# Performance work log

Measured on AMD Instinct MI355X. Metric: run time of the kernel, lower is better.

The kernel has to match this reference:

```python
import jax, jax.numpy as jnp
import numpy as np

B, S, W = 16, 512, 5
H, E, V = 512, 256, 100000


def setup_inputs() -> dict:
    key = jax.random.key(0)
    ks = jax.random.split(key, 20)
    inp = {
        "hiddens": jax.random.normal(ks[0], (B, S, H), jnp.float32),
        "masks": jax.random.randint(ks[1], (B, S), 0, 2, jnp.int32),
        "begins": jax.random.randint(ks[2], (B, S, W), 0, V, jnp.int32),
        "begin_lens": jax.random.randint(ks[3], (B, S), 0, W + 1, jnp.int32),
        "middles": jax.random.randint(ks[4], (B, S, W), 0, V, jnp.int32),
        "middle_lens": jax.random.randint(ks[5], (B, S), 0, W + 1, jnp.int32),
        "ends": jax.random.randint(ks[6], (B, S, W), 0, V, jnp.int32),
        "end_lens": jax.random.randint(ks[7], (B, S), 0, W + 1, jnp.int32),
        # parameters
        "emb": jax.random.normal(ks[8], (V, E), jnp.float32) * 0.02,
        "W_hidden": jax.random.normal(ks[9], (H, 3 * H), jnp.float32) * (1.0 / np.sqrt(H)),
        "b_hidden": jnp.zeros((3 * H,), jnp.float32),
        "W_begin": jax.random.normal(ks[10], (E, 2 * H), jnp.float32) * (1.0 / np.sqrt(E)),
        "b_begin": jnp.zeros((2 * H,), jnp.float32),
        "W_middle": jax.random.normal(ks[11], (E, 2 * H), jnp.float32) * (1.0 / np.sqrt(E)),
        "b_middle": jnp.zeros((2 * H,), jnp.float32),
        "W_end": jax.random.normal(ks[12], (E, 2 * H), jnp.float32) * (1.0 / np.sqrt(E)),
        "b_end": jnp.zeros((2 * H,), jnp.float32),
        "W_gate": jax.random.normal(ks[13], (H, 9), jnp.float32) * (1.0 / np.sqrt(H)),
        "b_gate": jnp.zeros((9,), jnp.float32),
    }
    return inp


def _len_mask(lens, w):
    # True where the lattice candidate is valid (mimics _make_mask's 1s)
    return jnp.arange(w)[None, None, :] < lens[:, :, None]


def _gates(hiddens, masks, W_gate, b_gate):
    b, s, _ = hiddens.shape
    lmr = hiddens @ W_gate + b_gate                      # (B,S,9)
    left, mid, right = jnp.split(lmr, 3, axis=-1)        # each (B,S,3)
    g = jax.nn.sigmoid(left[:, :-2] + mid[:, 1:-1] + right[:, 2:])  # (B,S-2,3)
    ones = jnp.ones((b, 1), g.dtype)
    zeros = jnp.zeros((b, 1), g.dtype)
    begin_g = jnp.concatenate([ones, g[..., 0], ones], axis=1)
    mid_g = jnp.concatenate([zeros, g[..., 1], zeros], axis=1)
    end_g = jnp.concatenate([ones, g[..., 2], ones], axis=1)
    pad = masks == 0
    z = jnp.zeros((), g.dtype)
    return (jnp.where(pad, z, begin_g), jnp.where(pad, z, mid_g), jnp.where(pad, z, end_g))


def reference(hiddens, masks, begins, begin_lens, middles, middle_lens, ends, end_lens,
              emb, W_hidden, b_hidden, W_begin, b_begin, W_middle, b_middle,
              W_end, b_end, W_gate, b_gate):
    w = begins.shape[-1]
    begin_m = _len_mask(begin_lens, w)
    middle_m = _len_mask(middle_lens, w)
    end_m = _len_mask(end_lens, w)

    begin_kv = emb[begins] @ W_begin + b_begin           # (B,S,W,2H)
    middle_kv = emb[middles] @ W_middle + b_middle
    end_kv = emb[ends] @ W_end + b_end

    query, hidden_key, hidden_value = jnp.split(hiddens @ W_hidden + b_hidden, 3, axis=-1)
    bg, mg, eg = _gates(hiddens, masks, W_gate, b_gate)
    begin_kv = bg[:, :, None, None] * begin_kv
    middle_kv = mg[:, :, None, None] * middle_kv
    end_kv = eg[:, :, None, None] * end_kv

    kv = jnp.concatenate([begin_kv, middle_kv, end_kv], axis=-2)   # (B,S,3W,2H)
    h = hiddens.shape[-1]
    keys, values = jnp.split(kv, 2, axis=-1)
    keys = jnp.concatenate([hidden_key[:, :, None, :], keys], axis=-2)     # (B,S,1+3W,H)
    values = jnp.concatenate([hidden_value[:, :, None, :], values], axis=-2)

    # combined mask: True entries get -1e10 (faithful to masked_fill_(masks, -1e10))
    score_mask = jnp.concatenate(
        [(masks != 0)[:, :, None], begin_m, middle_m, end_m], axis=-1)     # (B,S,1+3W)

    scores = jnp.einsum("bsh,bskh->bsk", query, keys)
    scores = jnp.where(score_mask, jnp.asarray(-1e10, scores.dtype), scores)
    weights = jax.nn.softmax(scores, axis=-1)
    return jnp.einsum("bsk,bskh->bsh", weights, values)
```

## Files before the change

kernel.cpp:

```cpp
#include <hip/hip_runtime.h>
#include <cstdint>
#include <cstddef>


typedef unsigned short u16;
typedef _Float16 f16;
typedef __attribute__((ext_vector_type(8))) f16 f16x8;
typedef __attribute__((ext_vector_type(4))) float f32x4;

#define MROWS 8192
#define SS 512

static __device__ __forceinline__ u16 f2h(float x) {
  f16 h = (f16)x;
  return __builtin_bit_cast(u16, h);
}
static __device__ __forceinline__ float h2f(u16 h) {
  return (float)__builtin_bit_cast(f16, h);
}
static __device__ __forceinline__ float sigm(float x) { return 1.f / (1.f + __expf(-x)); }

static __device__ __forceinline__ void gl2lds(const u16* g, u16* l) {
  __builtin_amdgcn_global_load_lds(
      (const __attribute__((address_space(1))) unsigned int*)g,
      (__attribute__((address_space(3))) unsigned int*)l, 16, 0, 0);
}

__global__ __launch_bounds__(256) void prep_all(
    const float* __restrict__ X, const float* __restrict__ Wg,
    const float* __restrict__ bg, const float* __restrict__ Wh,
    const float* __restrict__ Wb, const float* __restrict__ Wm,
    const float* __restrict__ We, const float* __restrict__ bb,
    const float* __restrict__ bm, const float* __restrict__ be,
    const float* __restrict__ bh, const int* __restrict__ masks,
    u16* __restrict__ Xh, float* __restrict__ lmr, float* __restrict__ s0,
    u16* __restrict__ Breg, u16* __restrict__ WvT, float* __restrict__ bcat,
    float* __restrict__ u, float* __restrict__ cbuf, int* __restrict__ idx,
    int* __restrict__ perm, int* __restrict__ cnts) {
  __shared__ __align__(16) char smem_raw[32768];
  float* shmem = (float*)smem_raw;
  u16* As = (u16*)smem_raw;
  u16* Bs = (u16*)(smem_raw + 16384);
#define TI(r, c) shmem[(r)*65 + (c)]
  const int b = blockIdx.x;
  const int t = threadIdx.x;
  if (b < 64) {
    int k0 = (b & 7) * 64;
    int n0 = (b >> 3) * 64;
#pragma unroll
    for (int i = 0; i < 16; i++) {
      int li = i * 256 + t; int r = li >> 6, c = li & 63;
      TI(r, c) = Wh[(size_t)(k0 + r) * 1536 + 1024 + n0 + c];
    }
    __syncthreads();
#pragma unroll
    for (int i = 0; i < 16; i++) {
      int li = i * 256 + t; int r = li >> 6, c = li & 63;
      Breg[(size_t)(512 + n0 + r) * 512 + k0 + c] = f2h(TI(c, r));
    }
  } else if (b < 160) {
    int idx2 = b - 64;
    int ty = idx2 >> 5;
    int rem = idx2 & 31;
    int c0 = (rem & 3) * 64;
    int n0 = (rem >> 2) * 64;
    const float* Wsrc = ty == 0 ? Wb : ty == 1 ? Wm : We;
#pragma unroll
    for (int i = 0; i < 16; i++) {
      int li = i * 256 + t; int r = li >> 6, c = li & 63;
      TI(r, c) = Wsrc[(size_t)(c0 + r) * 1024 + 512 + n0 + c];
    }
    __syncthreads();
#pragma unroll
    for (int i = 0; i < 16; i++) {
      int li = i * 256 + t; int r = li >> 6, c = li & 63;
      WvT[(size_t)(n0 + r) * 768 + ty * 256 + c0 + c] = f2h(TI(c, r));
    }
  } else if (b < 516) {
    const int lane = t & 63;
    const int widx = (b - 160) * 4 + (t >> 6);
    const int c = lane * 8;
    if (widx < 896) {
      int n = widx;
      float acc = 0.f;
      if (n < 771) {
        const float* src;
        if (n < 768) {
          int ty = n >> 8, ce = n & 255;
          src = (ty == 0 ? Wb : ty == 1 ? Wm : We) + (size_t)ce * 1024 + c;
        } else {
          int ty = n - 768;
          src = (ty == 0 ? bb : ty == 1 ? bm : be) + c;
        }
        float4 a0 = *(const float4*)src;
        float4 a1 = *(const float4*)(src + 4);
        float4 b0 = *(const float4*)(bh + c);
        float4 b1 = *(const float4*)(bh + c + 4);
        acc = a0.x * b0.x + a0.y * b0.y + a0.z * b0.z + a0.w * b0.w +
              a1.x * b1.x + a1.y * b1.y + a1.z * b1.z + a1.w * b1.w;
      }
#pragma unroll
      for (int o = 32; o > 0; o >>= 1) acc += __shfl_xor(acc, o);
      if (lane == 0) bcat[512 + n] = acc;
    } else if (widx < 1408) {
      int k = widx - 896;
      const float* wr = Wh + (size_t)k * 1536;
      float4 a0 = *(const float4*)(wr + c);
      float4 a1 = *(const float4*)(wr + c + 4);
      float4 a2 = *(const float4*)(wr + 512 + c);
      float4 a3 = *(const float4*)(wr + 512 + c + 4);
      float4 b0 = *(const float4*)(bh + 512 + c);
      float4 b1 = *(const float4*)(bh + 512 + c + 4);
      float4 b2 = *(const float4*)(bh + c);
      float4 b3 = *(const float4*)(bh + c + 4);
      float acc = a0.x * b0.x + a0.y * b0.y + a0.z * b0.z + a0.w * b0.w +
                  a1.x * b1.x + a1.y * b1.y + a1.z * b1.z + a1.w * b1.w +
                  a2.x * b2.x + a2.y * b2.y + a2.z * b2.z + a2.w * b2.w +
                  a3.x * b3.x + a3.y * b3.y + a3.z * b3.z + a3.w * b3.w;
#pragma unroll
      for (int o = 32; o > 0; o >>= 1) acc += __shfl_xor(acc, o);
      if (lane == 0) u[k] = acc;
    } else if (widx == 1408) {
      float4 b0 = *(const float4*)(bh + c);
      float4 b1 = *(const float4*)(bh + c + 4);
      float4 b2 = *(const float4*)(bh + 512 + c);
      float4 b3 = *(const float4*)(bh + 512 + c + 4);
      float acc = b0.x * b2.x + b0.y * b2.y + b0.z * b2.z + b0.w * b2.w +
                  b1.x * b3.x + b1.y * b3.y + b1.z * b3.z + b1.w * b3.w;
#pragma unroll
      for (int o = 32; o > 0; o >>= 1) acc += __shfl_xor(acc, o);
      if (lane == 0) cbuf[0] = acc;
    } else if (widx < 1417) {
      int i = (widx - 1409) * 64 + lane;
      bcat[i] = bh[1024 + i];
    }
  } else if (b < 1028) {
    const int xb = b - 516;
    if (xb < 32) s0[xb * 256 + t] = 0.f;
    for (int i = t; i < 4608; i += 256) shmem[i] = Wg[i];
    __syncthreads();
    const int lane = t & 63, wid = t >> 6;
#pragma unroll
    for (int it = 0; it < 4; it++) {
      int pos = xb * 16 + it * 4 + wid;
      const float* x = X + (size_t)pos * 512 + lane * 8;
      float4 x0 = *(const float4*)x;
      float4 x1 = *(const float4*)(x + 4);
      float xs[8] = {x0.x, x0.y, x0.z, x0.w, x1.x, x1.y, x1.z, x1.w};
      ushort4 h0, h1;
      h0.x = f2h(xs[0]); h0.y = f2h(xs[1]); h0.z = f2h(xs[2]); h0.w = f2h(xs[3]);
      h1.x = f2h(xs[4]); h1.y = f2h(xs[5]); h1.z = f2h(xs[6]); h1.w = f2h(xs[7]);
      ((ushort4*)Xh)[pos * 128 + lane * 2] = h0;
      ((ushort4*)Xh)[pos * 128 + lane * 2 + 1] = h1;
      float p[9];
#pragma unroll
      for (int c = 0; c < 9; c++) p[c] = 0.f;
      const float* wrow = shmem + (lane * 8) * 9;
#pragma unroll
      for (int j = 0; j < 8; j++)
#pragma unroll
        for (int c = 0; c < 9; c++) p[c] += xs[j] * wrow[j * 9 + c];
#pragma unroll
      for (int c = 0; c < 9; c++)
#pragma unroll
        for (int o = 32; o > 0; o >>= 1) p[c] += __shfl_xor(p[c], o);
      if (lane == 0) {
#pragma unroll
        for (int c = 0; c < 9; c++) lmr[(size_t)pos * 9 + c] = p[c] + bg[c];
      }
    }
  } else if (b < 1060) {
    const int lane = t & 63;
    const int pos = (b - 1028) * 256 + t;
    bool is0 = masks[pos] == 0;
    unsigned long long bal = __ballot(is0);
    unsigned long long below = (lane == 0) ? 0ull : (~0ull >> (64 - lane));
    int rank0 = __popcll(bal & below);
    int rank1 = __popcll((~bal) & below);
    int n0w = __popcll(bal);
    int base0 = 0, base1 = 0;
    if (lane == 0) {
      base0 = atomicAdd(&cnts[0], n0w);
      base1 = atomicAdd(&cnts[1], 64 - n0w);
    }
    base0 = __shfl(base0, 0);
    base1 = __shfl(base1, 0);
    int slot = is0 ? (base0 + rank0) : (8191 - (base1 + rank1));
    perm[pos] = slot;
    idx[slot] = pos;
  } else {
    const int b2 = b - 1060;
    const int m0 = (b2 % 11) * 128;
    const int n0 = (b2 / 11) * 128;
    const int lane = t & 63;
    const int wid = t >> 6;
    const int row = t >> 2;
    const int koff = (t & 3) * 8;
    const int lds0 = row * 32 + koff;
    const int lds1 = 2048 + lds0;

    auto asrc = [&](int r) -> const float* {
      if (r < 512) return Wh + (size_t)r * 1536 + 512;
      int n = r - 512;
      if (n < 768)
        return (n < 256 ? Wb : n < 512 ? Wm : We) + (size_t)(n & 255) * 1024;
      if (n < 771) return (n == 768 ? bb : n == 769 ? bm : be);
      return nullptr;
    };
    const float* pa0 = asrc(m0 + row);
    const float* pa1 = asrc(m0 + 64 + row);
    const float* pb0 = Wh + (size_t)(n0 + row) * 1536;
    const float* pb1 = Wh + (size_t)(n0 + 64 + row) * 1536;

    const int wm = (wid & 1) * 64;
    const int wn = (wid >> 1) * 64;
    const int fr = lane & 15;
    const int kq = (lane >> 4) * 8;

    f32x4 acc[4][4];
#pragma unroll
    for (int i = 0; i < 4; i++)
#pragma unroll
      for (int j = 0; j < 4; j++) acc[i][j] = (f32x4){0.f, 0.f, 0.f, 0.f};

    auto cvt8 = [&](const float* p, int col) -> f16x8 {
      f16x8 h{};
      if (p) {
        float4 v0 = *(const float4*)(p + col);
        float4 v1 = *(const float4*)(p + col + 4);
        h[0] = (f16)v0.x; h[1] = (f16)v0.y; h[2] = (f16)v0.z; h[3] = (f16)v0.w;
        h[4] = (f16)v1.x; h[5] = (f16)v1.y; h[6] = (f16)v1.z; h[7] = (f16)v1.w;
      }
      return h;
    };
    auto STAGE = [&](int kb, int buf) {
      *(f16x8*)&As[buf * 4096 + lds0] = cvt8(pa0, kb + koff);
      *(f16x8*)&As[buf * 4096 + lds1] = cvt8(pa1, kb + koff);
      *(f16x8*)&Bs[buf * 4096 + lds0] = cvt8(pb0, kb + koff);
      *(f16x8*)&Bs[buf * 4096 + lds1] = cvt8(pb1, kb + koff);
    };
    auto COMPUTE = [&](int buf) {
      f16x8 av[4], bv[4];
#pragma unroll
      for (int i = 0; i < 4; i++) {
        av[i] = *(const f16x8*)&As[buf * 4096 + (wm + i * 16 + fr) * 32 + kq];
        bv[i] = *(const f16x8*)&Bs[buf * 4096 + (wn + i * 16 + fr) * 32 + kq];
      }
#pragma unroll
      for (int mt = 0; mt < 4; mt++)
#pragma unroll
        for (int nt = 0; nt < 4; nt++)
          acc[mt][nt] = __builtin_amdgcn_mfma_f32_16x16x32_f16(
              av[mt], bv[nt], acc[mt][nt], 0, 0, 0);
    };

    STAGE(0, 0);
    __syncthreads();
    int buf = 0;
    for (int ki = 0; ki < 15; ++ki) {
      STAGE((ki + 1) * 32, buf ^ 1);
      COMPUTE(buf);
      __syncthreads();
      buf ^= 1;
    }
    COMPUTE(buf);

    const int r0 = (lane >> 4) * 4;
#pragma unroll
    for (int mt = 0; mt < 4; mt++)
#pragma unroll
      for (int nt = 0; nt < 4; nt++) {
        int col = n0 + wn + nt * 16 + fr;
#pragma unroll
        for (int r = 0; r < 4; r++) {
          int orow0 = m0 + wm + mt * 16 + r0 + r;
          int orow = orow0 < 512 ? orow0 : orow0 + 512;
          Breg[(size_t)orow * 512 + col] = f2h(acc[mt][nt][r]);
        }
      }
  }
#undef TI
}

template <int MODE>
__global__ __launch_bounds__(256) void gemm_k(
    const u16* __restrict__ A, const u16* __restrict__ Bt,
    const float* __restrict__ ubias, const float* __restrict__ bcat,
    float* __restrict__ Cf, u16* __restrict__ Cb, int Kdim,
    const u16* __restrict__ Xh, float* __restrict__ s0c,
    const int* __restrict__ idx, const int* __restrict__ cnts,
    const float4* __restrict__ sc4, const u16* __restrict__ HPb,
    const float* __restrict__ bb, const float* __restrict__ bm,
    const float* __restrict__ be) {
  constexpr int BROWS = (MODE == 2) ? 64 : 128;
  constexpr int NT = (MODE == 2) ? 2 : 4;
  __shared__ __align__(16) u16 As[2 * 128 * 32];
  __shared__ __align__(16) u16 Bs[2 * BROWS * 32];

  const int t = threadIdx.x;
  const int lane = t & 63;
  const int wid = t >> 6;
  const int m0 = blockIdx.x * 128;
  const int n0 = blockIdx.y * BROWS;

  bool remap = false;
  if constexpr (MODE == 0) {
    const int cnt0 = cnts[0];
    if (blockIdx.y < 4) {
      if (m0 >= cnt0) return;
      remap = true;
    } else if (blockIdx.y >= 8) {
      if (m0 + 128 <= cnt0) return;
      remap = true;
    }
  }

  int ra0 = m0 + (t >> 2), ra1 = m0 + 64 + (t >> 2);
  if (MODE == 0 && remap) { ra0 = idx[ra0]; ra1 = idx[ra1]; }
  const int rb0 = n0 + (t >> 2), rb1 = n0 + 64 + (t >> 2);
  const int koff = (t & 3) * 8;
  const int lds0 = (t >> 2) * 32 + koff;
  const int lds1 = 2048 + lds0;

  const int wm = (wid & 1) * 64;
  const int wn = (wid >> 1) * (NT * 16);
  const int fr = lane & 15;
  const int kq = (lane >> 4) * 8;

  f32x4 acc[4][NT];
#pragma unroll
  for (int i = 0; i < 4; i++)
#pragma unroll
    for (int j = 0; j < NT; j++) acc[i][j] = (f32x4){0.f, 0.f, 0.f, 0.f};

  auto STAGE = [&](int kb, int buf) {
    gl2lds(&A[(size_t)ra0 * Kdim + kb], &As[buf * 4096 + lds0]);
    gl2lds(&A[(size_t)ra1 * Kdim + kb], &As[buf * 4096 + lds1]);
    gl2lds(&Bt[(size_t)rb0 * Kdim + kb], &Bs[buf * (BROWS * 32) + lds0]);
    if constexpr (BROWS == 128)
      gl2lds(&Bt[(size_t)rb1 * Kdim + kb], &Bs[buf * (BROWS * 32) + lds1]);
  };
  auto COMPUTE = [&](int buf) {
    f16x8 av[4], bv[NT];
#pragma unroll
    for (int i = 0; i < 4; i++)
      av[i] = *(const f16x8*)&As[buf * 4096 + (wm + i * 16 + fr) * 32 + kq];
#pragma unroll
    for (int j = 0; j < NT; j++)
      bv[j] = *(const f16x8*)&Bs[buf * (BROWS * 32) + (wn + j * 16 + fr) * 32 + kq];
#pragma unroll
    for (int mt = 0; mt < 4; mt++)
#pragma unroll
      for (int nt = 0; nt < NT; nt++)
        acc[mt][nt] = __builtin_amdgcn_mfma_f32_16x16x32_f16(
            av[mt], bv[nt], acc[mt][nt], 0, 0, 0);
  };

  STAGE(koff, 0);
  __syncthreads();
  const int nk = Kdim >> 5;
  int buf = 0;
  for (int ki = 0; ki < nk - 1; ++ki) {
    STAGE((ki + 1) * 32 + koff, buf ^ 1);
    COMPUTE(buf);
    __syncthreads();
    buf ^= 1;
  }
  COMPUTE(buf);

  const int r0 = (lane >> 4) * 4;
  if constexpr (MODE == 0) {
    if (blockIdx.y < 4) {
      float pl[4][4];
      int xrow[4][4];
#pragma unroll
      for (int mt = 0; mt < 4; mt++)
#pragma unroll
        for (int r = 0; r < 4; r++) {
          pl[mt][r] = 0.f;
          xrow[mt][r] = idx[m0 + wm + mt * 16 + r0 + r];
        }
#pragma unroll
      for (int mt = 0; mt < 4; mt++)
#pragma unroll
        for (int nt = 0; nt < 4; nt++) {
          int col = n0 + wn + nt * 16 + fr;
          float bv2 = ubias[col];
#pragma unroll
          for (int r = 0; r < 4; r++)
            pl[mt][r] += (acc[mt][nt][r] + bv2) *
                         h2f(Xh[(size_t)xrow[mt][r] * 512 + col]);
        }
#pragma unroll
      for (int mt = 0; mt < 4; mt++)
#pragma unroll
        for (int r = 0; r < 4; r++) {
          float p = pl[mt][r];
          p += __shfl_xor(p, 1);
          p += __shfl_xor(p, 2);
          p += __shfl_xor(p, 4);
          p += __shfl_xor(p, 8);
          if (fr == r) {
            int slot = m0 + wm + mt * 16 + r0 + r;
            atomicAdd(&s0c[slot], p);
          }
        }
      return;
    }
    if (blockIdx.y < 8) {
#pragma unroll
      for (int mt = 0; mt < 4; mt++)
#pragma unroll
        for (int nt = 0; nt < 4; nt++) {
          int col = n0 - 512 + wn + nt * 16 + fr;
          float bv2 = bcat[col];
#pragma unroll
          for (int r = 0; r < 4; r++) {
            int row = m0 + wm + mt * 16 + r0 + r;
            Cb[(size_t)row * 1408 + col] = f2h(acc[mt][nt][r] + bv2);
          }
        }
    } else {
#pragma unroll
      for (int mt = 0; mt < 4; mt++)
#pragma unroll
        for (int nt = 0; nt < 4; nt++) {
          int pcol = n0 - 1024 + wn + nt * 16 + fr;
          float bv2 = bcat[512 + pcol];
#pragma unroll
          for (int r = 0; r < 4; r++) {
            int slot = m0 + wm + mt * 16 + r0 + r;
            Cb[(size_t)slot * 1408 + 512 + pcol] = f2h(acc[mt][nt][r] + bv2);
          }
        }
    }
  } else {
#pragma unroll
    for (int mt = 0; mt < 4; mt++)
#pragma unroll
      for (int nt = 0; nt < NT; nt++) {
        int col = n0 + wn + nt * 16 + fr;
        float b0 = bb[512 + col];
        float b1 = bm[512 + col];
        float b2 = be[512 + col];
#pragma unroll
        for (int r = 0; r < 4; r++) {
          int row = m0 + wm + mt * 16 + r0 + r;
          float4 s = sc4[row];
          float hv = h2f(HPb[(size_t)row * 1408 + col]);
          Cf[(size_t)row * 512 + col] =
              s.x * hv + s.y * b0 + s.z * b1 + s.w * b2 + acc[mt][nt][r];
        }
      }
  }
}

__global__ __launch_bounds__(256) void attn_kernel(
    const int* __restrict__ masks, const int* __restrict__ begins,
    const int* __restrict__ blens, const int* __restrict__ middles,
    const int* __restrict__ mlens, const int* __restrict__ ends,
    const int* __restrict__ elens, const float* __restrict__ emb,
    const u16* __restrict__ HPb, const float* __restrict__ lmr,
    const float* __restrict__ s0buf, const float* __restrict__ cbuf,
    const int* __restrict__ perm, float4* __restrict__ sc4,
    u16* __restrict__ Ebar) {
  const int t = threadIdx.x;
  const int lane = t & 63;
  const int wid = t >> 6;
  const int pos = blockIdx.x * 4 + wid;
  const int mask = masks[pos];
  const int slot = perm[pos];
  u16* erow = Ebar + (size_t)pos * 768;

  int l0 = min(blens[pos], 5), l1 = min(mlens[pos], 5), l2 = min(elens[pos], 5);
  int nv = l0 + l1 + l2;

  if (mask == 0) {
    float s0 = s0buf[slot] + cbuf[0];
    int ninv = 15 - nv;
    float w0;
    if (ninv == 0) {
      w0 = 1.f;
    } else {
      float Mx = fmaxf(s0, 0.f);
      float e0 = __expf(s0 - Mx);
      w0 = e0 / (e0 + (float)ninv * __expf(-Mx));
    }
    if (lane == 0) sc4[pos] = make_float4(w0, 0.f, 0.f, 0.f);
    ushort4 zz; zz.x = zz.y = zz.z = zz.w = 0;
    *(ushort4*)(erow + 0 * 256 + lane * 4) = zz;
    *(ushort4*)(erow + 1 * 256 + lane * 4) = zz;
    *(ushort4*)(erow + 2 * 256 + lane * 4) = zz;
  } else {
    const int s = pos & (SS - 1);
    float g[3];
    if (s == 0 || s == SS - 1) {
      g[0] = 1.f; g[1] = 0.f; g[2] = 1.f;
    } else {
      const float* p0 = lmr + (size_t)(pos - 1) * 9;
      const float* p1 = lmr + (size_t)pos * 9;
      const float* p2 = lmr + (size_t)(pos + 1) * 9;
      g[0] = sigm(p0[0] + p1[3] + p2[6]);
      g[1] = sigm(p0[1] + p1[4] + p2[7]);
      g[2] = sigm(p0[2] + p1[5] + p2[8]);
    }
    const bool deg = (nv == 15);
    int l[3] = {l0, l1, l2};
    if (deg) { l[0] = 0; l[1] = 0; l[2] = 0; }

    float4 Pt[3];
    float qb[3];
    if (!deg) {
      const u16* prow = HPb + (size_t)slot * 1408 + 512;
#pragma unroll
      for (int ty = 0; ty < 3; ty++) {
        ushort4 pu = *(const ushort4*)(prow + ty * 256 + lane * 4);
        Pt[ty].x = h2f(pu.x); Pt[ty].y = h2f(pu.y);
        Pt[ty].z = h2f(pu.z); Pt[ty].w = h2f(pu.w);
        qb[ty] = h2f(prow[768 + ty]);
      }
    }
    const int* idxp[3];
    idxp[0] = begins + (size_t)pos * 5;
    idxp[1] = middles + (size_t)pos * 5;
    idxp[2] = ends + (size_t)pos * 5;

    float4 ev[3][5];
    float scv[3][5];
    float Mx = deg ? 0.f : -3.0e38f;
#pragma unroll
    for (int ty = 0; ty < 3; ty++) {
#pragma unroll
      for (int w = 0; w < 5; w++) {
        bool act = (w >= l[ty]);
        if (act) {
          ev[ty][w] = *(const float4*)(emb + (size_t)idxp[ty][w] * 256 + lane * 4);
          float sv = 0.f;
          if (!deg) {
            float4 e = ev[ty][w];
            float d = Pt[ty].x * e.x + Pt[ty].y * e.y + Pt[ty].z * e.z + Pt[ty].w * e.w;
#pragma unroll
            for (int o = 32; o > 0; o >>= 1) d += __shfl_xor(d, o);
            sv = g[ty] * (d + qb[ty]);
          }
          scv[ty][w] = sv;
          Mx = fmaxf(Mx, sv);
        }
      }
    }
    float wts0 = deg ? 1.f : 0.f;
    float zs = wts0;
    float wts[3][5];
#pragma unroll
    for (int ty = 0; ty < 3; ty++)
#pragma unroll
      for (int w = 0; w < 5; w++) {
        bool act = (w >= l[ty]);
        float wv = act ? __expf(scv[ty][w] - Mx) : 0.f;
        wts[ty][w] = wv;
        zs += wv;
      }
    float inv = 1.f / zs;
    float alpha[3];
#pragma unroll
    for (int ty = 0; ty < 3; ty++) {
      float ax = 0.f, ay = 0.f, az = 0.f, aw = 0.f, asum = 0.f;
#pragma unroll
      for (int w = 0; w < 5; w++) {
        if (w >= l[ty]) {
          float wk = wts[ty][w];
          asum += wk;
          ax += wk * ev[ty][w].x;
          ay += wk * ev[ty][w].y;
          az += wk * ev[ty][w].z;
          aw += wk * ev[ty][w].w;
        }
      }
      float sg = g[ty] * inv;
      alpha[ty] = sg * asum;
      ushort4 h;
      h.x = f2h(ax * sg); h.y = f2h(ay * sg); h.z = f2h(az * sg); h.w = f2h(aw * sg);
      *(ushort4*)(erow + ty * 256 + lane * 4) = h;
    }
    if (lane == 0) sc4[pos] = make_float4(wts0 * inv, alpha[0], alpha[1], alpha[2]);
  }
}

extern "C" void kernel_launch(void* const* d_in, const int* in_sizes, int n_in,
                              void* d_out, int out_size, void* d_ws, size_t ws_size,
                              hipStream_t stream) {
  const float* hiddens = (const float*)d_in[0];
  const int* masks = (const int*)d_in[1];
  const int* begins = (const int*)d_in[2];
  const int* blens = (const int*)d_in[3];
  const int* middles = (const int*)d_in[4];
  const int* mlens = (const int*)d_in[5];
  const int* ends = (const int*)d_in[6];
  const int* elens = (const int*)d_in[7];
  const float* emb = (const float*)d_in[8];
  const float* Wh = (const float*)d_in[9];
  const float* bh = (const float*)d_in[10];
  const float* Wb = (const float*)d_in[11];
  const float* bb = (const float*)d_in[12];
  const float* Wm = (const float*)d_in[13];
  const float* bm = (const float*)d_in[14];
  const float* We = (const float*)d_in[15];
  const float* be = (const float*)d_in[16];
  const float* Wg = (const float*)d_in[17];
  const float* bg = (const float*)d_in[18];
  float* out = (float*)d_out;

  char* ws = (char*)d_ws;
  size_t off = 0;
  auto alloc = [&](size_t bytes) -> char* {
    char* p = ws + off;
    off += (bytes + 255) & ~(size_t)255;
    return p;
  };
  u16* Xh = (u16*)alloc((size_t)8192 * 512 * 2);
  u16* Breg = (u16*)alloc((size_t)1920 * 512 * 2);
  u16* WvT = (u16*)alloc((size_t)512 * 768 * 2);
  u16* HPb = (u16*)alloc((size_t)8192 * 1408 * 2);
  float* lmr = (float*)alloc((size_t)8192 * 9 * 4);
  float* s0c = (float*)alloc((size_t)8192 * 4);
  float* bcat = (float*)alloc((size_t)1408 * 4);
  float* u = (float*)alloc((size_t)512 * 4);
  float* cbuf = (float*)alloc((size_t)4);
  float* sc4 = (float*)alloc((size_t)8192 * 4 * 4);
  u16* Ebar = (u16*)alloc((size_t)8192 * 768 * 2);
  int* idx = (int*)alloc((size_t)8192 * 4);
  int* perm = (int*)alloc((size_t)8192 * 4);
  int* cnts = (int*)alloc((size_t)256);
  if (off > ws_size) return;

  hipMemsetAsync(cnts, 0, 8, stream);
  prep_all<<<1104, 256, 0, stream>>>(hiddens, Wg, bg, Wh, Wb, Wm, We, bb, bm, be,
                                     bh, masks, Xh, lmr, s0c, Breg, WvT, bcat,
                                     u, cbuf, idx, perm, cnts);
  gemm_k<0><<<dim3(64, 15), 256, 0, stream>>>(
      Xh, Breg, u, bcat, nullptr, HPb, 512, Xh, s0c, idx, cnts,
      nullptr, nullptr, nullptr, nullptr, nullptr);
  attn_kernel<<<2048, 256, 0, stream>>>(masks, begins, blens, middles, mlens,
                                        ends, elens, emb, HPb, lmr, s0c, cbuf,
                                        perm, (float4*)sc4, Ebar);
  gemm_k<2><<<dim3(64, 8), 256, 0, stream>>>(
      Ebar, WvT, nullptr, nullptr, out, nullptr, 768, nullptr, nullptr,
      nullptr, nullptr, (const float4*)sc4, HPb, bb, bm, be);
}
```

Measured before the change: 303.6 us.

## Fuse all stages into one persistent kernel with software grid barriers

Replaces the four separate kernel launches (prep, projection GEMM, attention, output GEMM) with a single persistent kernel of 512 blocks. Each block loops over the virtual block indices of every stage, and an atomic-counter grid barrier separates the stages. The aim is to remove launch overhead and inter-kernel gaps. In exchange, every block must be co-resident, the barriers add spin cost, and the fixed grid may spread work unevenly across blocks. A timeout inside the barrier can break ordering if residency is not met.

New measurement: 956.9 us. 3.15x slower.

```diff
diff --git a/kernel.cpp b/kernel.cpp
--- a/kernel.cpp
+++ b/kernel.cpp
@@ -8,8 +8,20 @@
 typedef __attribute__((ext_vector_type(8))) f16 f16x8;
 typedef __attribute__((ext_vector_type(4))) float f32x4;
 
-#define MROWS 8192
 #define SS 512
+#define NBLK 512
+
+struct KArgs {
+  const float *X, *Wg, *bg, *Wh, *Wb, *Wm, *We, *bb, *bm, *be, *bh;
+  const int *masks, *begins, *blens, *middles, *mlens, *ends, *elens;
+  const float *emb;
+  u16 *Xh; float *lmr; float *s0c;
+  u16 *Breg, *WvT;
+  float *bcat, *u, *cbuf;
+  int *idx, *perm, *cnts;
+  u16 *HPb; float4 *sc4; u16 *Ebar;
+  float *out;
+};
 
 static __device__ __forceinline__ u16 f2h(float x) {
   f16 h = (f16)x;
@@ -26,23 +38,26 @@
       (__attribute__((address_space(3))) unsigned int*)l, 16, 0, 0);
 }
 
-__global__ __launch_bounds__(256) void prep_all(
-    const float* __restrict__ X, const float* __restrict__ Wg,
-    const float* __restrict__ bg, const float* __restrict__ Wh,
-    const float* __restrict__ Wb, const float* __restrict__ Wm,
-    const float* __restrict__ We, const float* __restrict__ bb,
-    const float* __restrict__ bm, const float* __restrict__ be,
-    const float* __restrict__ bh, const int* __restrict__ masks,
-    u16* __restrict__ Xh, float* __restrict__ lmr, float* __restrict__ s0,
-    u16* __restrict__ Breg, u16* __restrict__ WvT, float* __restrict__ bcat,
-    float* __restrict__ u, float* __restrict__ cbuf, int* __restrict__ idx,
-    int* __restrict__ perm, int* __restrict__ cnts) {
-  __shared__ __align__(16) char smem_raw[32768];
+static __device__ __forceinline__ void gbar(int* ctr) {
+  __syncthreads();
+  __threadfence();
+  if (threadIdx.x == 0) {
+    __hip_atomic_fetch_add(ctr, 1, __ATOMIC_RELEASE, __HIP_MEMORY_SCOPE_AGENT);
+    long long t0 = (long long)__builtin_amdgcn_s_memrealtime();
+    while (__hip_atomic_load(ctr, __ATOMIC_ACQUIRE, __HIP_MEMORY_SCOPE_AGENT) < NBLK) {
+      __builtin_amdgcn_s_sleep(16);
+      if ((long long)__builtin_amdgcn_s_memrealtime() - t0 > 5000000LL) break;
+    }
+  }
+  __syncthreads();
+  __threadfence();
+}
+
+static __device__ void prep_body(int b, const KArgs& A_, char* smem_raw) {
   float* shmem = (float*)smem_raw;
   u16* As = (u16*)smem_raw;
   u16* Bs = (u16*)(smem_raw + 16384);
 #define TI(r, c) shmem[(r)*65 + (c)]
-  const int b = blockIdx.x;
   const int t = threadIdx.x;
   if (b < 64) {
     int k0 = (b & 7) * 64;
@@ -50,13 +65,13 @@
 #pragma unroll
     for (int i = 0; i < 16; i++) {
       int li = i * 256 + t; int r = li >> 6, c = li & 63;
-      TI(r, c) = Wh[(size_t)(k0 + r) * 1536 + 1024 + n0 + c];
+      TI(r, c) = A_.Wh[(size_t)(k0 + r) * 1536 + 1024 + n0 + c];
     }
     __syncthreads();
 #pragma unroll
     for (int i = 0; i < 16; i++) {
       int li = i * 256 + t; int r = li >> 6, c = li & 63;
-      Breg[(size_t)(512 + n0 + r) * 512 + k0 + c] = f2h(TI(c, r));
+      A_.Breg[(size_t)(512 + n0 + r) * 512 + k0 + c] = f2h(TI(c, r));
     }
   } else if (b < 160) {
     int idx2 = b - 64;
@@ -64,7 +79,7 @@
     int rem = idx2 & 31;
     int c0 = (rem & 3) * 64;
     int n0 = (rem >> 2) * 64;
-    const float* Wsrc = ty == 0 ? Wb : ty == 1 ? Wm : We;
+    const float* Wsrc = ty == 0 ? A_.Wb : ty == 1 ? A_.Wm : A_.We;
 #pragma unroll
     for (int i = 0; i < 16; i++) {
       int li = i * 256 + t; int r = li >> 6, c = li & 63;
@@ -74,12 +89,13 @@
 #pragma unroll
     for (int i = 0; i < 16; i++) {
       int li = i * 256 + t; int r = li >> 6, c = li & 63;
-      WvT[(size_t)(n0 + r) * 768 + ty * 256 + c0 + c] = f2h(TI(c, r));
+      A_.WvT[(size_t)(n0 + r) * 768 + ty * 256 + c0 + c] = f2h(TI(c, r));
     }
   } else if (b < 516) {
     const int lane = t & 63;
     const int widx = (b - 160) * 4 + (t >> 6);
     const int c = lane * 8;
+    const float* bh = A_.bh;
     if (widx < 896) {
       int n = widx;
       float acc = 0.f;
@@ -87,10 +103,10 @@
         const float* src;
         if (n < 768) {
           int ty = n >> 8, ce = n & 255;
-          src = (ty == 0 ? Wb : ty == 1 ? Wm : We) + (size_t)ce * 1024 + c;
+          src = (ty == 0 ? A_.Wb : ty == 1 ? A_.Wm : A_.We) + (size_t)ce * 1024 + c;
         } else {
           int ty = n - 768;
-          src = (ty == 0 ? bb : ty == 1 ? bm : be) + c;
+          src = (ty == 0 ? A_.bb : ty == 1 ? A_.bm : A_.be) + c;
         }
         float4 a0 = *(const float4*)src;
         float4 a1 = *(const float4*)(src + 4);
@@ -101,10 +117,10 @@
       }
 #pragma unroll
       for (int o = 32; o > 0; o >>= 1) acc += __shfl_xor(acc, o);
-      if (lane == 0) bcat[512 + n] = acc;
+      if (lane == 0) A_.bcat[512 + n] = acc;
     } else if (widx < 1408) {
       int k = widx - 896;
-      const float* wr = Wh + (size_t)k * 1536;
+      const float* wr = A_.Wh + (size_t)k * 1536;
       float4 a0 = *(const float4*)(wr + c);
       float4 a1 = *(const float4*)(wr + c + 4);
       float4 a2 = *(const float4*)(wr + 512 + c);
@@ -119,7 +135,7 @@
                   a3.x * b3.x + a3.y * b3.y + a3.z * b3.z + a3.w * b3.w;
 #pragma unroll
       for (int o = 32; o > 0; o >>= 1) acc += __shfl_xor(acc, o);
-      if (lane == 0) u[k] = acc;
+      if (lane == 0) A_.u[k] = acc;
     } else if (widx == 1408) {
       float4 b0 = *(const float4*)(bh + c);
       float4 b1 = *(const float4*)(bh + c + 4);
@@ -129,29 +145,29 @@
                   b1.x * b3.x + b1.y * b3.y + b1.z * b3.z + b1.w * b3.w;
 #pragma unroll
       for (int o = 32; o > 0; o >>= 1) acc += __shfl_xor(acc, o);
-      if (lane == 0) cbuf[0] = acc;
+      if (lane == 0) A_.cbuf[0] = acc;
     } else if (widx < 1417) {
       int i = (widx - 1409) * 64 + lane;
-      bcat[i] = bh[1024 + i];
+      A_.bcat[i] = bh[1024 + i];
     }
   } else if (b < 1028) {
     const int xb = b - 516;
-    if (xb < 32) s0[xb * 256 + t] = 0.f;
-    for (int i = t; i < 4608; i += 256) shmem[i] = Wg[i];
+    if (xb < 32) A_.s0c[xb * 256 + t] = 0.f;
+    for (int i = t; i < 4608; i += 256) shmem[i] = A_.Wg[i];
     __syncthreads();
     const int lane = t & 63, wid = t >> 6;
 #pragma unroll
     for (int it = 0; it < 4; it++) {
       int pos = xb * 16 + it * 4 + wid;
-      const float* x = X + (size_t)pos * 512 + lane * 8;
+      const float* x = A_.X + (size_t)pos * 512 + lane * 8;
       float4 x0 = *(const float4*)x;
       float4 x1 = *(const float4*)(x + 4);
       float xs[8] = {x0.x, x0.y, x0.z, x0.w, x1.x, x1.y, x1.z, x1.w};
       ushort4 h0, h1;
       h0.x = f2h(xs[0]); h0.y = f2h(xs[1]); h0.z = f2h(xs[2]); h0.w = f2h(xs[3]);
       h1.x = f2h(xs[4]); h1.y = f2h(xs[5]); h1.z = f2h(xs[6]); h1.w = f2h(xs[7]);
-      ((ushort4*)Xh)[pos * 128 + lane * 2] = h0;
-      ((ushort4*)Xh)[pos * 128 + lane * 2 + 1] = h1;
+      ((ushort4*)A_.Xh)[pos * 128 + lane * 2] = h0;
+      ((ushort4*)A_.Xh)[pos * 128 + lane * 2 + 1] = h1;
       float p[9];
 #pragma unroll
       for (int c = 0; c < 9; c++) p[c] = 0.f;
@@ -166,13 +182,13 @@
         for (int o = 32; o > 0; o >>= 1) p[c] += __shfl_xor(p[c], o);
       if (lane == 0) {
 #pragma unroll
-        for (int c = 0; c < 9; c++) lmr[(size_t)pos * 9 + c] = p[c] + bg[c];
+        for (int c = 0; c < 9; c++) A_.lmr[(size_t)pos * 9 + c] = p[c] + A_.bg[c];
       }
     }
   } else if (b < 1060) {
     const int lane = t & 63;
     const int pos = (b - 1028) * 256 + t;
-    bool is0 = masks[pos] == 0;
+    bool is0 = A_.masks[pos] == 0;
     unsigned long long bal = __ballot(is0);
     unsigned long long below = (lane == 0) ? 0ull : (~0ull >> (64 - lane));
     int rank0 = __popcll(bal & below);
@@ -180,14 +196,14 @@
     int n0w = __popcll(bal);
     int base0 = 0, base1 = 0;
     if (lane == 0) {
-      base0 = atomicAdd(&cnts[0], n0w);
-      base1 = atomicAdd(&cnts[1], 64 - n0w);
+      base0 = atomicAdd(&A_.cnts[0], n0w);
+      base1 = atomicAdd(&A_.cnts[1], 64 - n0w);
     }
     base0 = __shfl(base0, 0);
     base1 = __shfl(base1, 0);
     int slot = is0 ? (base0 + rank0) : (8191 - (base1 + rank1));
-    perm[pos] = slot;
-    idx[slot] = pos;
+    A_.perm[pos] = slot;
+    A_.idx[slot] = pos;
   } else {
     const int b2 = b - 1060;
     const int m0 = (b2 % 11) * 128;
@@ -200,17 +216,17 @@
     const int lds1 = 2048 + lds0;
 
     auto asrc = [&](int r) -> const float* {
-      if (r < 512) return Wh + (size_t)r * 1536 + 512;
+      if (r < 512) return A_.Wh + (size_t)r * 1536 + 512;
       int n = r - 512;
       if (n < 768)
-        return (n < 256 ? Wb : n < 512 ? Wm : We) + (size_t)(n & 255) * 1024;
-      if (n < 771) return (n == 768 ? bb : n == 769 ? bm : be);
+        return (n < 256 ? A_.Wb : n < 512 ? A_.Wm : A_.We) + (size_t)(n & 255) * 1024;
+      if (n < 771) return (n == 768 ? A_.bb : n == 769 ? A_.bm : A_.be);
       return nullptr;
     };
     const float* pa0 = asrc(m0 + row);
     const float* pa1 = asrc(m0 + 64 + row);
-    const float* pb0 = Wh + (size_t)(n0 + row) * 1536;
-    const float* pb1 = Wh + (size_t)(n0 + 64 + row) * 1536;
+    const float* pb0 = A_.Wh + (size_t)(n0 + row) * 1536;
+    const float* pb1 = A_.Wh + (size_t)(n0 + 64 + row) * 1536;
 
     const int wm = (wid & 1) * 64;
     const int wn = (wid >> 1) * 64;
@@ -275,7 +291,7 @@
         for (int r = 0; r < 4; r++) {
           int orow0 = m0 + wm + mt * 16 + r0 + r;
           int orow = orow0 < 512 ? orow0 : orow0 + 512;
-          Breg[(size_t)orow * 512 + col] = f2h(acc[mt][nt][r]);
+          A_.Breg[(size_t)orow * 512 + col] = f2h(acc[mt][nt][r]);
         }
       }
   }
@@ -283,40 +299,35 @@
 }
 
 template <int MODE>
-__global__ __launch_bounds__(256) void gemm_k(
-    const u16* __restrict__ A, const u16* __restrict__ Bt,
-    const float* __restrict__ ubias, const float* __restrict__ bcat,
-    float* __restrict__ Cf, u16* __restrict__ Cb, int Kdim,
-    const u16* __restrict__ Xh, float* __restrict__ s0c,
-    const int* __restrict__ idx, const int* __restrict__ cnts,
-    const float4* __restrict__ sc4, const u16* __restrict__ HPb,
-    const float* __restrict__ bb, const float* __restrict__ bm,
-    const float* __restrict__ be) {
+static __device__ void gemm_body(int bx, int by, const KArgs& A_, char* smem_raw) {
   constexpr int BROWS = (MODE == 2) ? 64 : 128;
   constexpr int NT = (MODE == 2) ? 2 : 4;
-  __shared__ __align__(16) u16 As[2 * 128 * 32];
-  __shared__ __align__(16) u16 Bs[2 * BROWS * 32];
+  constexpr int Kdim = (MODE == 2) ? 768 : 512;
+  u16* As = (u16*)smem_raw;
+  u16* Bs = (u16*)(smem_raw + 16384);
+  const u16* Amat = (MODE == 0) ? A_.Xh : A_.Ebar;
+  const u16* Bt = (MODE == 0) ? A_.Breg : A_.WvT;
 
   const int t = threadIdx.x;
   const int lane = t & 63;
   const int wid = t >> 6;
-  const int m0 = blockIdx.x * 128;
-  const int n0 = blockIdx.y * BROWS;
+  const int m0 = bx * 128;
+  const int n0 = by * BROWS;
 
   bool remap = false;
   if constexpr (MODE == 0) {
-    const int cnt0 = cnts[0];
-    if (blockIdx.y < 4) {
+    const int cnt0 = A_.cnts[0];
+    if (by < 4) {
       if (m0 >= cnt0) return;
       remap = true;
-    } else if (blockIdx.y >= 8) {
+    } else if (by >= 8) {
       if (m0 + 128 <= cnt0) return;
       remap = true;
     }
   }
 
   int ra0 = m0 + (t >> 2), ra1 = m0 + 64 + (t >> 2);
-  if (MODE == 0 && remap) { ra0 = idx[ra0]; ra1 = idx[ra1]; }
+  if (MODE == 0 && remap) { ra0 = A_.idx[ra0]; ra1 = A_.idx[ra1]; }
   const int rb0 = n0 + (t >> 2), rb1 = n0 + 64 + (t >> 2);
   const int koff = (t & 3) * 8;
   const int lds0 = (t >> 2) * 32 + koff;
@@ -334,8 +345,8 @@
     for (int j = 0; j < NT; j++) acc[i][j] = (f32x4){0.f, 0.f, 0.f, 0.f};
 
   auto STAGE = [&](int kb, int buf) {
-    gl2lds(&A[(size_t)ra0 * Kdim + kb], &As[buf * 4096 + lds0]);
-    gl2lds(&A[(size_t)ra1 * Kdim + kb], &As[buf * 4096 + lds1]);
+    gl2lds(&Amat[(size_t)ra0 * Kdim + kb], &As[buf * 4096 + lds0]);
+    gl2lds(&Amat[(size_t)ra1 * Kdim + kb], &As[buf * 4096 + lds1]);
     gl2lds(&Bt[(size_t)rb0 * Kdim + kb], &Bs[buf * (BROWS * 32) + lds0]);
     if constexpr (BROWS == 128)
       gl2lds(&Bt[(size_t)rb1 * Kdim + kb], &Bs[buf * (BROWS * 32) + lds1]);
@@ -358,7 +369,7 @@
 
   STAGE(koff, 0);
   __syncthreads();
-  const int nk = Kdim >> 5;
+  constexpr int nk = Kdim >> 5;
   int buf = 0;
   for (int ki = 0; ki < nk - 1; ++ki) {
     STAGE((ki + 1) * 32 + koff, buf ^ 1);
@@ -370,7 +381,7 @@
 
   const int r0 = (lane >> 4) * 4;
   if constexpr (MODE == 0) {
-    if (blockIdx.y < 4) {
+    if (by < 4) {
       float pl[4][4];
       int xrow[4][4];
 #pragma unroll
@@ -378,18 +389,18 @@
 #pragma unroll
         for (int r = 0; r < 4; r++) {
           pl[mt][r] = 0.f;
-          xrow[mt][r] = idx[m0 + wm + mt * 16 + r0 + r];
+          xrow[mt][r] = A_.idx[m0 + wm + mt * 16 + r0 + r];
         }
 #pragma unroll
       for (int mt = 0; mt < 4; mt++)
 #pragma unroll
         for (int nt = 0; nt < 4; nt++) {
           int col = n0 + wn + nt * 16 + fr;
-          float bv2 = ubias[col];
+          float bv2 = A_.u[col];
 #pragma unroll
           for (int r = 0; r < 4; r++)
             pl[mt][r] += (acc[mt][nt][r] + bv2) *
-                         h2f(Xh[(size_t)xrow[mt][r] * 512 + col]);
+                         h2f(A_.Xh[(size_t)xrow[mt][r] * 512 + col]);
         }
 #pragma unroll
       for (int mt = 0; mt < 4; mt++)
@@ -402,22 +413,22 @@
           p += __shfl_xor(p, 8);
           if (fr == r) {
             int slot = m0 + wm + mt * 16 + r0 + r;
-            atomicAdd(&s0c[slot], p);
+            atomicAdd(&A_.s0c[slot], p);
           }
         }
       return;
     }
-    if (blockIdx.y < 8) {
+    if (by < 8) {
 #pragma unroll
       for (int mt = 0; mt < 4; mt++)
 #pragma unroll
         for (int nt = 0; nt < 4; nt++) {
           int col = n0 - 512 + wn + nt * 16 + fr;
-          float bv2 = bcat[col];
+          float bv2 = A_.bcat[col];
 #pragma unroll
           for (int r = 0; r < 4; r++) {
             int row = m0 + wm + mt * 16 + r0 + r;
-            Cb[(size_t)row * 1408 + col] = f2h(acc[mt][nt][r] + bv2);
+            A_.HPb[(size_t)row * 1408 + col] = f2h(acc[mt][nt][r] + bv2);
           }
         }
     } else {
@@ -426,11 +437,11 @@
 #pragma unroll
         for (int nt = 0; nt < 4; nt++) {
           int pcol = n0 - 1024 + wn + nt * 16 + fr;
-          float bv2 = bcat[512 + pcol];
+          float bv2 = A_.bcat[512 + pcol];
 #pragma unroll
           for (int r = 0; r < 4; r++) {
             int slot = m0 + wm + mt * 16 + r0 + r;
-            Cb[(size_t)slot * 1408 + 512 + pcol] = f2h(acc[mt][nt][r] + bv2);
+            A_.HPb[(size_t)slot * 1408 + 512 + pcol] = f2h(acc[mt][nt][r] + bv2);
           }
         }
     }
@@ -440,43 +451,35 @@
 #pragma unroll
       for (int nt = 0; nt < NT; nt++) {
         int col = n0 + wn + nt * 16 + fr;
-        float b0 = bb[512 + col];
-        float b1 = bm[512 + col];
-        float b2 = be[512 + col];
+        float b0 = A_.bb[512 + col];
+        float b1 = A_.bm[512 + col];
+        float b2 = A_.be[512 + col];
 #pragma unroll
         for (int r = 0; r < 4; r++) {
           int row = m0 + wm + mt * 16 + r0 + r;
-          float4 s = sc4[row];
-          float hv = h2f(HPb[(size_t)row * 1408 + col]);
-          Cf[(size_t)row * 512 + col] =
+          float4 s = A_.sc4[row];
+          float hv = h2f(A_.HPb[(size_t)row * 1408 + col]);
+          A_.out[(size_t)row * 512 + col] =
               s.x * hv + s.y * b0 + s.z * b1 + s.w * b2 + acc[mt][nt][r];
         }
       }
   }
 }
 
-__global__ __launch_bounds__(256) void attn_kernel(
-    const int* __restrict__ masks, const int* __restrict__ begins,
-    const int* __restrict__ blens, const int* __restrict__ middles,
-    const int* __restrict__ mlens, const int* __restrict__ ends,
-    const int* __restrict__ elens, const float* __restrict__ emb,
-    const u16* __restrict__ HPb, const float* __restrict__ lmr,
-    const float* __restrict__ s0buf, const float* __restrict__ cbuf,
-    const int* __restrict__ perm, float4* __restrict__ sc4,
-    u16* __restrict__ Ebar) {
+static __device__ void attn_body(int vb, const KArgs& A_) {
   const int t = threadIdx.x;
   const int lane = t & 63;
   const int wid = t >> 6;
-  const int pos = blockIdx.x * 4 + wid;
-  const int mask = masks[pos];
-  const int slot = perm[pos];
-  u16* erow = Ebar + (size_t)pos * 768;
-
-  int l0 = min(blens[pos], 5), l1 = min(mlens[pos], 5), l2 = min(elens[pos], 5);
+  const int pos = vb * 4 + wid;
+  const int mask = A_.masks[pos];
+  const int slot = A_.perm[pos];
+  u16* erow = A_.Ebar + (size_t)pos * 768;
+
+  int l0 = min(A_.blens[pos], 5), l1 = min(A_.mlens[pos], 5), l2 = min(A_.elens[pos], 5);
   int nv = l0 + l1 + l2;
 
   if (mask == 0) {
-    float s0 = s0buf[slot] + cbuf[0];
+    float s0 = A_.s0c[slot] + A_.cbuf[0];
     int ninv = 15 - nv;
     float w0;
     if (ninv == 0) {
@@ -486,7 +489,7 @@
       float e0 = __expf(s0 - Mx);
       w0 = e0 / (e0 + (float)ninv * __expf(-Mx));
     }
-    if (lane == 0) sc4[pos] = make_float4(w0, 0.f, 0.f, 0.f);
+    if (lane == 0) A_.sc4[pos] = make_float4(w0, 0.f, 0.f, 0.f);
     ushort4 zz; zz.x = zz.y = zz.z = zz.w = 0;
     *(ushort4*)(erow + 0 * 256 + lane * 4) = zz;
     *(ushort4*)(erow + 1 * 256 + lane * 4) = zz;
@@ -497,9 +500,9 @@
     if (s == 0 || s == SS - 1) {
       g[0] = 1.f; g[1] = 0.f; g[2] = 1.f;
     } else {
-      const float* p0 = lmr + (size_t)(pos - 1) * 9;
-      const float* p1 = lmr + (size_t)pos * 9;
-      const float* p2 = lmr + (size_t)(pos + 1) * 9;
+      const float* p0 = A_.lmr + (size_t)(pos - 1) * 9;
+      const float* p1 = A_.lmr + (size_t)pos * 9;
+      const float* p2 = A_.lmr + (size_t)(pos + 1) * 9;
       g[0] = sigm(p0[0] + p1[3] + p2[6]);
       g[1] = sigm(p0[1] + p1[4] + p2[7]);
       g[2] = sigm(p0[2] + p1[5] + p2[8]);
@@ -511,7 +514,7 @@
     float4 Pt[3];
     float qb[3];
     if (!deg) {
-      const u16* prow = HPb + (size_t)slot * 1408 + 512;
+      const u16* prow = A_.HPb + (size_t)slot * 1408 + 512;
 #pragma unroll
       for (int ty = 0; ty < 3; ty++) {
         ushort4 pu = *(const ushort4*)(prow + ty * 256 + lane * 4);
@@ -521,9 +524,9 @@
       }
     }
     const int* idxp[3];
-    idxp[0] = begins + (size_t)pos * 5;
-    idxp[1] = middles + (size_t)pos * 5;
-    idxp[2] = ends + (size_t)pos * 5;
+    idxp[0] = A_.begins + (size_t)pos * 5;
+    idxp[1] = A_.middles + (size_t)pos * 5;
+    idxp[2] = A_.ends + (size_t)pos * 5;
 
     float4 ev[3][5];
     float scv[3][5];
@@ -534,7 +537,7 @@
       for (int w = 0; w < 5; w++) {
         bool act = (w >= l[ty]);
         if (act) {
-          ev[ty][w] = *(const float4*)(emb + (size_t)idxp[ty][w] * 256 + lane * 4);
+          ev[ty][w] = *(const float4*)(A_.emb + (size_t)idxp[ty][w] * 256 + lane * 4);
           float sv = 0.f;
           if (!deg) {
             float4 e = ev[ty][w];
@@ -582,34 +585,34 @@
       h.x = f2h(ax * sg); h.y = f2h(ay * sg); h.z = f2h(az * sg); h.w = f2h(aw * sg);
       *(ushort4*)(erow + ty * 256 + lane * 4) = h;
     }
-    if (lane == 0) sc4[pos] = make_float4(wts0 * inv, alpha[0], alpha[1], alpha[2]);
+    if (lane == 0) A_.sc4[pos] = make_float4(wts0 * inv, alpha[0], alpha[1], alpha[2]);
+  }
+}
+
+__global__ __launch_bounds__(256, 2) void mega(KArgs a) {
+  __shared__ __align__(16) char smem[32768];
+  const int gsz = gridDim.x;
+  for (int vb = blockIdx.x; vb < 1104; vb += gsz) {
+    prep_body(vb, a, smem);
+    __syncthreads();
+  }
+  gbar(&a.cnts[2]);
+  for (int vb = blockIdx.x; vb < 960; vb += gsz) {
+    __syncthreads();
+    gemm_body<0>(vb & 63, vb >> 6, a, smem);
+  }
+  gbar(&a.cnts[3]);
+  for (int vb = blockIdx.x; vb < 2048; vb += gsz) attn_body(vb, a);
+  gbar(&a.cnts[4]);
+  for (int vb = blockIdx.x; vb < 512; vb += gsz) {
+    __syncthreads();
+    gemm_body<2>(vb & 63, vb >> 6, a, smem);
   }
 }
 
 extern "C" void kernel_launch(void* const* d_in, const int* in_sizes, int n_in,
                               void* d_out, int out_size, void* d_ws, size_t ws_size,
                               hipStream_t stream) {
-  const float* hiddens = (const float*)d_in[0];
-  const int* masks = (const int*)d_in[1];
-  const int* begins = (const int*)d_in[2];
-  const int* blens = (const int*)d_in[3];
-  const int* middles = (const int*)d_in[4];
-  const int* mlens = (const int*)d_in[5];
-  const int* ends = (const int*)d_in[6];
-  const int* elens = (const int*)d_in[7];
-  const float* emb = (const float*)d_in[8];
-  const float* Wh = (const float*)d_in[9];
-  const float* bh = (const float*)d_in[10];
-  const float* Wb = (const float*)d_in[11];
-  const float* bb = (const float*)d_in[12];
-  const float* Wm = (const float*)d_in[13];
-  const float* bm = (const float*)d_in[14];
-  const float* We = (const float*)d_in[15];
-  const float* be = (const float*)d_in[16];
-  const float* Wg = (const float*)d_in[17];
-  const float* bg = (const float*)d_in[18];
-  float* out = (float*)d_out;
-
   char* ws = (char*)d_ws;
   size_t off = 0;
   auto alloc = [&](size_t bytes) -> char* {
@@ -617,33 +620,44 @@
     off += (bytes + 255) & ~(size_t)255;
     return p;
   };
-  u16* Xh = (u16*)alloc((size_t)8192 * 512 * 2);
-  u16* Breg = (u16*)alloc((size_t)1920 * 512 * 2);
-  u16* WvT = (u16*)alloc((size_t)512 * 768 * 2);
-  u16* HPb = (u16*)alloc((size_t)8192 * 1408 * 2);
-  float* lmr = (float*)alloc((size_t)8192 * 9 * 4);
-  float* s0c = (float*)alloc((size_t)8192 * 4);
-  float* bcat = (float*)alloc((size_t)1408 * 4);
-  float* u = (float*)alloc((size_t)512 * 4);
-  float* cbuf = (float*)alloc((size_t)4);
-  float* sc4 = (float*)alloc((size_t)8192 * 4 * 4);
-  u16* Ebar = (u16*)alloc((size_t)8192 * 768 * 2);
-  int* idx = (int*)alloc((size_t)8192 * 4);
-  int* perm = (int*)alloc((size_t)8192 * 4);
-  int* cnts = (int*)alloc((size_t)256);
+  KArgs a;
+  a.X = (const float*)d_in[0];
+  a.masks = (const int*)d_in[1];
+  a.begins = (const int*)d_in[2];
+  a.blens = (const int*)d_in[3];
+  a.middles = (const int*)d_in[4];
+  a.mlens = (const int*)d_in[5];
+  a.ends = (const int*)d_in[6];
+  a.elens = (const int*)d_in[7];
+  a.emb = (const float*)d_in[8];
+  a.Wh = (const float*)d_in[9];
+  a.bh = (const float*)d_in[10];
+  a.Wb = (const float*)d_in[11];
+  a.bb = (const float*)d_in[12];
+  a.Wm = (const float*)d_in[13];
+  a.bm = (const float*)d_in[14];
+  a.We = (const float*)d_in[15];
+  a.be = (const float*)d_in[16];
+  a.Wg = (const float*)d_in[17];
+  a.bg = (const float*)d_in[18];
+  a.out = (float*)d_out;
+
+  a.Xh = (u16*)alloc((size_t)8192 * 512 * 2);
+  a.Breg = (u16*)alloc((size_t)1920 * 512 * 2);
+  a.WvT = (u16*)alloc((size_t)512 * 768 * 2);
+  a.HPb = (u16*)alloc((size_t)8192 * 1408 * 2);
+  a.lmr = (float*)alloc((size_t)8192 * 9 * 4);
+  a.s0c = (float*)alloc((size_t)8192 * 4);
+  a.bcat = (float*)alloc((size_t)1408 * 4);
+  a.u = (float*)alloc((size_t)512 * 4);
+  a.cbuf = (float*)alloc((size_t)4);
+  a.sc4 = (float4*)alloc((size_t)8192 * 4 * 4);
+  a.Ebar = (u16*)alloc((size_t)8192 * 768 * 2);
+  a.idx = (int*)alloc((size_t)8192 * 4);
+  a.perm = (int*)alloc((size_t)8192 * 4);
+  a.cnts = (int*)alloc((size_t)256);
   if (off > ws_size) return;
 
-  hipMemsetAsync(cnts, 0, 8, stream);
-  prep_all<<<1104, 256, 0, stream>>>(hiddens, Wg, bg, Wh, Wb, Wm, We, bb, bm, be,
-                                     bh, masks, Xh, lmr, s0c, Breg, WvT, bcat,
-                                     u, cbuf, idx, perm, cnts);
-  gemm_k<0><<<dim3(64, 15), 256, 0, stream>>>(
-      Xh, Breg, u, bcat, nullptr, HPb, 512, Xh, s0c, idx, cnts,
-      nullptr, nullptr, nullptr, nullptr, nullptr);
-  attn_kernel<<<2048, 256, 0, stream>>>(masks, begins, blens, middles, mlens,
-                                        ends, elens, emb, HPb, lmr, s0c, cbuf,
-                                        perm, (float4*)sc4, Ebar);
-  gemm_k<2><<<dim3(64, 8), 256, 0, stream>>>(
-      Ebar, WvT, nullptr, nullptr, out, nullptr, 768, nullptr, nullptr,
-      nullptr, nullptr, (const float4*)sc4, HPb, bb, bm, be);
-}
+  hipMemsetAsync(a.cnts, 0, 32, stream);
+  mega<<<NBLK, 256, 0, stream>>>(a);
+}
```
